# Kernel optimization log

Measured on AMD Instinct MI355X. Metric: run time of the kernel, lower is better.

Reference implementation:

```python
import jax, jax.numpy as jnp
import numpy as np

N = 100000   # nodes
E = 1600000  # edges
DIN, H, DOUT = 128, 64, 40
EPS = 1e-5

def setup_inputs() -> dict:
    key = jax.random.key(0)
    ks = jax.random.split(key, 8)
    def w(k, fan_in, shape):
        return jax.random.normal(k, shape, jnp.float32) * (1.0 / np.sqrt(fan_in))
    return {
        "node_feat": jax.random.normal(ks[0], (N, DIN), jnp.float32),
        "edge_index": jax.random.randint(ks[1], (2, E), 0, N, dtype=jnp.int32),
        "W1": w(ks[2], DIN, (DIN, H)), "b1": jnp.zeros((H,), jnp.float32),
        "g1": jnp.ones((H,), jnp.float32), "beta1": jnp.zeros((H,), jnp.float32),
        "W2": w(ks[3], H, (H, H)), "b2": jnp.zeros((H,), jnp.float32),
        "g2": jnp.ones((H,), jnp.float32), "beta2": jnp.zeros((H,), jnp.float32),
        "W3": w(ks[4], H, (H, H)), "b3": jnp.zeros((H,), jnp.float32),
        "Wf": w(ks[5], H, (H, DOUT)), "bf": jnp.zeros((DOUT,), jnp.float32),
    }

def _gcn_conv(x, src, dst, norm, W, b):
    # x: [N, Cin] -> linear then D^{-1/2}(A+I)D^{-1/2} aggregation (PyG GCNConv)
    h = x @ W                              # [N, Cout]
    msg = h[src] * norm[:, None]           # [E+N, Cout] gather + scale
    return jax.ops.segment_sum(msg, dst, num_segments=N) + b

def _bn(x, g, b):
    # BatchNorm1d over node dim with batch statistics (biased var)
    m = jnp.mean(x, axis=0)
    v = jnp.mean((x - m) ** 2, axis=0)
    return (x - m) * jax.lax.rsqrt(v + EPS) * g + b

def reference(node_feat, edge_index, W1, b1, g1, beta1, W2, b2, g2, beta2, W3, b3, Wf, bf):
    loop = jnp.arange(N, dtype=edge_index.dtype)
    src = jnp.concatenate([edge_index[0], loop])   # add self loops
    dst = jnp.concatenate([edge_index[1], loop])
    deg = jax.ops.segment_sum(jnp.ones_like(src, dtype=node_feat.dtype), dst, num_segments=N)
    dis = jax.lax.rsqrt(deg)                        # deg >= 1 (self loops)
    norm = dis[src] * dis[dst]                      # [E+N]

    x1 = jax.nn.relu(_bn(_gcn_conv(node_feat, src, dst, norm, W1, b1), g1, beta1))
    # dropout is identity in eval mode
    x2 = jax.nn.relu(_bn(_gcn_conv(x1, src, dst, norm, W2, b2), g2, beta2))
    x3 = _gcn_conv(x2, src, dst, norm, W3, b3)

    x = jnp.max(jnp.stack([x1, x2, x3], axis=0), axis=0)  # JumpingKnowledge 'max'
    return x @ Wf + bf
```

## Files before the change

kernel.cpp:

```cpp
#include <hip/hip_runtime.h>

#define NN 100000
#define NE 1600000
#define DIN 128
#define HDIM 64
#define DOUT 40
#define EPS 1e-5f
#define NXCD 8
#define CAP 64

typedef int int4v __attribute__((ext_vector_type(4)));
typedef float f4v __attribute__((ext_vector_type(4)));

__device__ __forceinline__ float bf2f(unsigned short v) {
    return __uint_as_float(((unsigned int)v) << 16);
}
__device__ __forceinline__ unsigned short f2bf(float f) {
    unsigned int u = __float_as_uint(f);
    u += 0x7FFFu + ((u >> 16) & 1u);
    return (unsigned short)(u >> 16);
}

__device__ __forceinline__ int ntl(const int* p) { return __builtin_nontemporal_load(p); }
__device__ __forceinline__ int4v ntl4(const int4v* p) { return __builtin_nontemporal_load(p); }
__device__ __forceinline__ f4v ntlf4(const f4v* p) { return __builtin_nontemporal_load(p); }

__global__ __launch_bounds__(256) void fill_kernel(const int* __restrict__ ei,
                                                   int* __restrict__ cnt,
                                                   int* __restrict__ esrc) {
    const int xcd = blockIdx.x & (NXCD - 1);
    const int lo = xcd * (NN / NXCD);
    const int hi = (xcd == NXCD - 1) ? NN : lo + (NN / NXCD);
    const int slot = blockIdx.x >> 3;
    const int nslot = gridDim.x >> 3;
    const int4v* d4 = (const int4v*)(ei + NE);
    for (int e4 = slot * blockDim.x + threadIdx.x; e4 < NE / 4; e4 += nslot * blockDim.x) {
        int4v d = ntl4(d4 + e4);
#pragma unroll
        for (int k = 0; k < 4; ++k) {
            int dd = d[k];
            if (dd >= lo && dd < hi) {
                int pos = atomicAdd(&cnt[dd], 1);
                if (pos < CAP) {
                    int s = ntl(ei + 4 * e4 + k);
                    __builtin_nontemporal_store(s, &esrc[(dd << 6) + pos]);
                }
            }
        }
    }
}

__global__ __launch_bounds__(256) void dis_kernel(const int* __restrict__ cnt,
                                                  float* __restrict__ dis) {
    for (int i = blockIdx.x * blockDim.x + threadIdx.x; i < NN; i += gridDim.x * blockDim.x)
        dis[i] = rsqrtf((float)(cnt[i] + 1));
}

template <int K, int TR, bool BN, bool NTL>
__global__ __launch_bounds__(256) void gemm_lds(const float* __restrict__ x,
                                                const float* __restrict__ W,
                                                const float* __restrict__ dis,
                                                const float* __restrict__ sc,
                                                const float* __restrict__ sh,
                                                unsigned short* __restrict__ h2) {
    __shared__ float xs[TR][K];
    const int tid = threadIdx.x;
    const int lane = tid & 63;
    const int wv = tid >> 6;
    float w[K];
#pragma unroll
    for (int k = 0; k < K; ++k) w[k] = W[k * 64 + lane];

    float4 scv, shv;
    if (BN) {
        const int c4 = tid & (K / 4 - 1);
        scv = ((const float4*)sc)[c4];
        shv = ((const float4*)sh)[c4];
    }

    const int row0 = blockIdx.x * TR;
    const int remRows = NN - row0;
    const int nvec = ((remRows >= TR) ? TR : remRows) * K / 4;
    const f4v* srcv = (const f4v*)(x + (long long)row0 * K);
    f4v* dstv = (f4v*)&xs[0][0];
    for (int i = tid; i < nvec; i += 256) {
        f4v v = NTL ? ntlf4(srcv + i) : srcv[i];
        if (BN) {
            v.x = fmaxf(fmaf(v.x, scv.x, shv.x), 0.f);
            v.y = fmaxf(fmaf(v.y, scv.y, shv.y), 0.f);
            v.z = fmaxf(fmaf(v.z, scv.z, shv.z), 0.f);
            v.w = fmaxf(fmaf(v.w, scv.w, shv.w), 0.f);
        }
        dstv[i] = v;
    }
    __syncthreads();

    const int rpw = TR / 4;
#pragma unroll
    for (int rr = 0; rr < rpw; ++rr) {
        const int r = wv * rpw + rr;
        const int row = row0 + r;
        if (row >= NN) break;
        float a0 = 0.f, a1 = 0.f, a2 = 0.f, a3 = 0.f;
#pragma unroll
        for (int k = 0; k < K; k += 4) {
            float4 xv = *(const float4*)&xs[r][k];
            a0 = fmaf(xv.x, w[k + 0], a0);
            a1 = fmaf(xv.y, w[k + 1], a1);
            a2 = fmaf(xv.z, w[k + 2], a2);
            a3 = fmaf(xv.w, w[k + 3], a3);
        }
        h2[row * 64 + lane] = f2bf(((a0 + a1) + (a2 + a3)) * dis[row]);
    }
}

__global__ __launch_bounds__(256) void agg_csr(const int* __restrict__ cnt,
                                               const int* __restrict__ esrc,
                                               const float* __restrict__ dis,
                                               const unsigned short* __restrict__ h2,
                                               float* __restrict__ y) {
    const int tid = threadIdx.x;
    const int wv = tid >> 6;
    const int lane = tid & 63;
    const int half = lane >> 5;
    const int c = lane & 31;
    const int node = blockIdx.x * 8 + wv * 2 + half;
    const ushort2* h2v = (const ushort2*)h2;
    ushort2 p0 = h2v[node * 32 + c];
    float ax = bf2f(p0.x), ay = bf2f(p0.y);
    const int deg = min(cnt[node], CAP);
    const int m = max(deg, __shfl_xor(deg, 32));
    const int jb = node << 6;
#pragma unroll 8
    for (int t = 0; t < m; ++t) {
        int sv = esrc[jb + t];
        int s = (t < deg) ? sv : NN;
        ushort2 p = h2v[s * 32 + c];
        ax += bf2f(p.x);
        ay += bf2f(p.y);
    }
    float dn = dis[node];
    ((float2*)(y + node * 64))[c] = make_float2(ax * dn, ay * dn);
}

__global__ __launch_bounds__(256) void agg_final(const int* __restrict__ cnt,
                                                 const int* __restrict__ esrc,
                                                 const float* __restrict__ dis,
                                                 const unsigned short* __restrict__ h2,
                                                 const float* __restrict__ x1,
                                                 const float* __restrict__ x2,
                                                 const float* __restrict__ sc1,
                                                 const float* __restrict__ sh1,
                                                 const float* __restrict__ sc2,
                                                 const float* __restrict__ sh2,
                                                 const float* __restrict__ b3,
                                                 const float* __restrict__ Wf,
                                                 const float* __restrict__ bf,
                                                 float* __restrict__ out) {
    __shared__ float m[8][64];
    const int tid = threadIdx.x;
    const int wv = tid >> 6;
    const int lane = tid & 63;
    const int half = lane >> 5;
    const int c = lane & 31;
    const int node = blockIdx.x * 8 + wv * 2 + half;
    const ushort2* h2v = (const ushort2*)h2;
    ushort2 p0 = h2v[node * 32 + c];
    float ax = bf2f(p0.x), ay = bf2f(p0.y);
    const int deg = min(cnt[node], CAP);
    const int mm = max(deg, __shfl_xor(deg, 32));
    const int jb = node << 6;
#pragma unroll 8
    for (int t = 0; t < mm; ++t) {
        int sv = esrc[jb + t];
        int s = (t < deg) ? sv : NN;
        ushort2 p = h2v[s * 32 + c];
        ax += bf2f(p.x);
        ay += bf2f(p.y);
    }
    const float dn = dis[node];
    const int c0 = 2 * c;
    const int o = node * 64 + c0;
    float2 x1v = *(const float2*)(x1 + o);
    float2 x2v = *(const float2*)(x2 + o);
    float v3x = fmaf(ax, dn, b3[c0]);
    float v3y = fmaf(ay, dn, b3[c0 + 1]);
    float v1x = fmaxf(fmaf(x1v.x, sc1[c0], sh1[c0]), 0.f);
    float v1y = fmaxf(fmaf(x1v.y, sc1[c0 + 1], sh1[c0 + 1]), 0.f);
    float v2x = fmaxf(fmaf(x2v.x, sc2[c0], sh2[c0]), 0.f);
    float v2y = fmaxf(fmaf(x2v.y, sc2[c0 + 1], sh2[c0 + 1]), 0.f);
    const int rl = wv * 2 + half;
    m[rl][c0] = fmaxf(fmaxf(v1x, v2x), v3x);
    m[rl][c0 + 1] = fmaxf(fmaxf(v1y, v2y), v3y);
    __syncthreads();
#pragma unroll
    for (int rr = wv; rr < 8; rr += 4) {
        if (lane < DOUT) {
            float a2 = bf[lane];
#pragma unroll
            for (int k = 0; k < 64; ++k) a2 += m[rr][k] * Wf[k * DOUT + lane];
            out[(blockIdx.x * 8 + rr) * DOUT + lane] = a2;
        }
    }
}

__global__ __launch_bounds__(256) void stats_kernel(const float* __restrict__ y, float* stats) {
    const int tid = threadIdx.x;
    const int c = tid & 63, rg = tid >> 6;
    float s = 0.f, s2 = 0.f;
    for (int row = blockIdx.x * 4 + rg; row < NN; row += gridDim.x * 4) {
        float v = y[row * 64 + c];
        s += v;
        s2 += v * v;
    }
    __shared__ float ls[256], ls2[256];
    ls[tid] = s; ls2[tid] = s2;
    __syncthreads();
    if (tid < 64) {
        s = ls[tid] + ls[tid + 64] + ls[tid + 128] + ls[tid + 192];
        s2 = ls2[tid] + ls2[tid + 64] + ls2[tid + 128] + ls2[tid + 192];
        atomicAdd(&stats[tid], s);
        atomicAdd(&stats[64 + tid], s2);
    }
}

__global__ __launch_bounds__(64) void bn_coef(const float* __restrict__ stats,
                                              const float* __restrict__ g,
                                              const float* __restrict__ beta,
                                              float* __restrict__ sc,
                                              float* __restrict__ sh) {
    const int c = threadIdx.x;
    const float invN = 1.0f / NN;
    float m = stats[c] * invN;
    float var = stats[64 + c] * invN - m * m;
    float s = g[c] * rsqrtf(var + EPS);
    sc[c] = s;
    sh[c] = beta[c] - m * s;
}

extern "C" void kernel_launch(void* const* d_in, const int* in_sizes, int n_in,
                              void* d_out, int out_size, void* d_ws, size_t ws_size,
                              hipStream_t stream) {
    const float* node_feat = (const float*)d_in[0];
    const int*   ei        = (const int*)d_in[1];
    const float* W1 = (const float*)d_in[2];
    const float* g1 = (const float*)d_in[4];
    const float* beta1 = (const float*)d_in[5];
    const float* W2 = (const float*)d_in[6];
    const float* g2 = (const float*)d_in[8];
    const float* beta2 = (const float*)d_in[9];
    const float* W3 = (const float*)d_in[10];
    const float* b3 = (const float*)d_in[11];
    const float* Wf = (const float*)d_in[12];
    const float* bf = (const float*)d_in[13];
    float* out = (float*)d_out;

    float* ws  = (float*)d_ws;
    float* dis = ws;
    unsigned short* h2 = (unsigned short*)(dis + NN);
    float* x1  = (float*)(h2 + (NN + 1) * 64);
    float* x2  = x1 + NN * 64;
    float* stats = x2 + NN * 64;
    float* sc1 = stats + 128;
    float* sh1 = sc1 + 64;
    float* sc2 = sh1 + 64;
    float* sh2 = sc2 + 64;
    int* cnt  = (int*)(sh2 + 64);
    int* esrc = cnt + NN;

    const int B = 256;
    const int gElem = 2048;
    const int gAgg = NN / 8;

    hipMemsetAsync(cnt, 0, NN * sizeof(int), stream);
    hipMemsetAsync(h2 + NN * 64, 0, 64 * sizeof(unsigned short), stream);
    fill_kernel<<<gElem, B, 0, stream>>>(ei, cnt, esrc);
    dis_kernel<<<512, B, 0, stream>>>(cnt, dis);

    gemm_lds<DIN, 32, false, true><<<(NN + 31) / 32, B, 0, stream>>>(node_feat, W1, dis, nullptr, nullptr, h2);
    agg_csr<<<gAgg, B, 0, stream>>>(cnt, esrc, dis, h2, x1);
    hipMemsetAsync(stats, 0, 128 * sizeof(float), stream);
    stats_kernel<<<512, B, 0, stream>>>(x1, stats);
    bn_coef<<<1, 64, 0, stream>>>(stats, g1, beta1, sc1, sh1);

    gemm_lds<HDIM, 64, true, false><<<(NN + 63) / 64, B, 0, stream>>>(x1, W2, dis, sc1, sh1, h2);
    agg_csr<<<gAgg, B, 0, stream>>>(cnt, esrc, dis, h2, x2);
    hipMemsetAsync(stats, 0, 128 * sizeof(float), stream);
    stats_kernel<<<512, B, 0, stream>>>(x2, stats);
    bn_coef<<<1, 64, 0, stream>>>(stats, g2, beta2, sc2, sh2);

    gemm_lds<HDIM, 64, true, false><<<(NN + 63) / 64, B, 0, stream>>>(x2, W3, dis, sc2, sh2, h2);
    agg_final<<<gAgg, B, 0, stream>>>(cnt, esrc, dis, h2, x1, x2,
                                      sc1, sh1, sc2, sh2, b3, Wf, bf, out);
}
```

Baseline: 428.7 us.

## Shard bf16 feature table into four column slices to shrink gather working set

The GEMM now writes h2 as four separate 16-column shards, and the aggregation kernels run four blocks per node group, each gathering only one shard. Each block's random gathers then touch a table a quarter the size, which is meant to improve cache hit rates (L2/MALL) for the irregular neighbour reads. The fused final layer is split out into a separate JK-max kernel that writes a jk buffer and a final projection kernel. The cost is more blocks that each re-read the edge lists (four times the index traffic) and an extra round trip through jk in memory.

```diff
diff --git a/kernel.cpp b/kernel.cpp
--- a/kernel.cpp
+++ b/kernel.cpp
@@ -8,6 +8,8 @@
 #define EPS 1e-5f
 #define NXCD 8
 #define CAP 64
+#define NSH 4
+#define SSTR ((NN + 1) * 16)
 
 typedef int int4v __attribute__((ext_vector_type(4)));
 typedef float f4v __attribute__((ext_vector_type(4)));
@@ -95,6 +97,7 @@
     }
     __syncthreads();
 
+    unsigned short* hout = h2 + (lane >> 4) * SSTR + (lane & 15);
     const int rpw = TR / 4;
 #pragma unroll
     for (int rr = 0; rr < rpw; ++rr) {
@@ -110,7 +113,7 @@
             a2 = fmaf(xv.z, w[k + 2], a2);
             a3 = fmaf(xv.w, w[k + 3], a3);
         }
-        h2[row * 64 + lane] = f2bf(((a0 + a1) + (a2 + a3)) * dis[row]);
+        hout[row * 16] = f2bf(((a0 + a1) + (a2 + a3)) * dis[row]);
     }
 }
 
@@ -120,87 +123,98 @@
                                                const unsigned short* __restrict__ h2,
                                                float* __restrict__ y) {
     const int tid = threadIdx.x;
+    const int g = blockIdx.x & (NSH - 1);
+    const int blk = blockIdx.x >> 2;
     const int wv = tid >> 6;
     const int lane = tid & 63;
-    const int half = lane >> 5;
-    const int c = lane & 31;
-    const int node = blockIdx.x * 8 + wv * 2 + half;
-    const ushort2* h2v = (const ushort2*)h2;
-    ushort2 p0 = h2v[node * 32 + c];
+    const int node = blk * 32 + wv * 8 + (lane >> 3);
+    const int cp = lane & 7;
+    const ushort2* hv = (const ushort2*)(h2 + g * SSTR);
+    ushort2 p0 = hv[node * 8 + cp];
     float ax = bf2f(p0.x), ay = bf2f(p0.y);
     const int deg = min(cnt[node], CAP);
-    const int m = max(deg, __shfl_xor(deg, 32));
+    int m = deg;
+    m = max(m, __shfl_xor(m, 8));
+    m = max(m, __shfl_xor(m, 16));
+    m = max(m, __shfl_xor(m, 32));
     const int jb = node << 6;
 #pragma unroll 8
     for (int t = 0; t < m; ++t) {
         int sv = esrc[jb + t];
         int s = (t < deg) ? sv : NN;
-        ushort2 p = h2v[s * 32 + c];
+        ushort2 p = hv[s * 8 + cp];
         ax += bf2f(p.x);
         ay += bf2f(p.y);
     }
     float dn = dis[node];
-    ((float2*)(y + node * 64))[c] = make_float2(ax * dn, ay * dn);
-}
-
-__global__ __launch_bounds__(256) void agg_final(const int* __restrict__ cnt,
-                                                 const int* __restrict__ esrc,
-                                                 const float* __restrict__ dis,
-                                                 const unsigned short* __restrict__ h2,
-                                                 const float* __restrict__ x1,
-                                                 const float* __restrict__ x2,
-                                                 const float* __restrict__ sc1,
-                                                 const float* __restrict__ sh1,
-                                                 const float* __restrict__ sc2,
-                                                 const float* __restrict__ sh2,
-                                                 const float* __restrict__ b3,
-                                                 const float* __restrict__ Wf,
-                                                 const float* __restrict__ bf,
-                                                 float* __restrict__ out) {
-    __shared__ float m[8][64];
-    const int tid = threadIdx.x;
+    ((float2*)(y + node * 64))[g * 8 + cp] = make_float2(ax * dn, ay * dn);
+}
+
+__global__ __launch_bounds__(256) void agg3_jk(const int* __restrict__ cnt,
+                                               const int* __restrict__ esrc,
+                                               const float* __restrict__ dis,
+                                               const unsigned short* __restrict__ h2,
+                                               const float* __restrict__ x1,
+                                               const float* __restrict__ x2,
+                                               const float* __restrict__ sc1,
+                                               const float* __restrict__ sh1,
+                                               const float* __restrict__ sc2,
+                                               const float* __restrict__ sh2,
+                                               const float* __restrict__ b3,
+                                               float* __restrict__ jk) {
+    const int tid = threadIdx.x;
+    const int g = blockIdx.x & (NSH - 1);
+    const int blk = blockIdx.x >> 2;
     const int wv = tid >> 6;
     const int lane = tid & 63;
-    const int half = lane >> 5;
-    const int c = lane & 31;
-    const int node = blockIdx.x * 8 + wv * 2 + half;
-    const ushort2* h2v = (const ushort2*)h2;
-    ushort2 p0 = h2v[node * 32 + c];
+    const int node = blk * 32 + wv * 8 + (lane >> 3);
+    const int cp = lane & 7;
+    const ushort2* hv = (const ushort2*)(h2 + g * SSTR);
+    ushort2 p0 = hv[node * 8 + cp];
     float ax = bf2f(p0.x), ay = bf2f(p0.y);
     const int deg = min(cnt[node], CAP);
-    const int mm = max(deg, __shfl_xor(deg, 32));
+    int m = deg;
+    m = max(m, __shfl_xor(m, 8));
+    m = max(m, __shfl_xor(m, 16));
+    m = max(m, __shfl_xor(m, 32));
     const int jb = node << 6;
 #pragma unroll 8
-    for (int t = 0; t < mm; ++t) {
+    for (int t = 0; t < m; ++t) {
         int sv = esrc[jb + t];
         int s = (t < deg) ? sv : NN;
-        ushort2 p = h2v[s * 32 + c];
+        ushort2 p = hv[s * 8 + cp];
         ax += bf2f(p.x);
         ay += bf2f(p.y);
     }
     const float dn = dis[node];
-    const int c0 = 2 * c;
-    const int o = node * 64 + c0;
-    float2 x1v = *(const float2*)(x1 + o);
-    float2 x2v = *(const float2*)(x2 + o);
+    const int c0 = g * 16 + cp * 2;
+    float2 x1v = ((const float2*)(x1 + node * 64))[g * 8 + cp];
+    float2 x2v = ((const float2*)(x2 + node * 64))[g * 8 + cp];
     float v3x = fmaf(ax, dn, b3[c0]);
     float v3y = fmaf(ay, dn, b3[c0 + 1]);
     float v1x = fmaxf(fmaf(x1v.x, sc1[c0], sh1[c0]), 0.f);
     float v1y = fmaxf(fmaf(x1v.y, sc1[c0 + 1], sh1[c0 + 1]), 0.f);
     float v2x = fmaxf(fmaf(x2v.x, sc2[c0], sh2[c0]), 0.f);
     float v2y = fmaxf(fmaf(x2v.y, sc2[c0 + 1], sh2[c0 + 1]), 0.f);
-    const int rl = wv * 2 + half;
-    m[rl][c0] = fmaxf(fmaxf(v1x, v2x), v3x);
-    m[rl][c0 + 1] = fmaxf(fmaxf(v1y, v2y), v3y);
+    ((float2*)(jk + node * 64))[g * 8 + cp] =
+        make_float2(fmaxf(fmaxf(v1x, v2x), v3x), fmaxf(fmaxf(v1y, v2y), v3y));
+}
+
+__global__ __launch_bounds__(256) void final_kernel(const float* __restrict__ jk,
+                                                    const float* __restrict__ Wf,
+                                                    const float* __restrict__ bf,
+                                                    float* __restrict__ out) {
+    __shared__ float m[4][64];
+    const int tid = threadIdx.x;
+    const int r = tid >> 6, c = tid & 63;
+    const int row = blockIdx.x * 4 + r;
+    m[r][c] = jk[row * 64 + c];
     __syncthreads();
-#pragma unroll
-    for (int rr = wv; rr < 8; rr += 4) {
-        if (lane < DOUT) {
-            float a2 = bf[lane];
-#pragma unroll
-            for (int k = 0; k < 64; ++k) a2 += m[rr][k] * Wf[k * DOUT + lane];
-            out[(blockIdx.x * 8 + rr) * DOUT + lane] = a2;
-        }
+    if (c < DOUT) {
+        float acc = bf[c];
+#pragma unroll
+        for (int k = 0; k < 64; ++k) acc += m[r][k] * Wf[k * DOUT + c];
+        out[row * DOUT + c] = acc;
     }
 }
 
@@ -258,9 +272,10 @@
     float* ws  = (float*)d_ws;
     float* dis = ws;
     unsigned short* h2 = (unsigned short*)(dis + NN);
-    float* x1  = (float*)(h2 + (NN + 1) * 64);
+    float* x1  = (float*)(h2 + NSH * SSTR);
     float* x2  = x1 + NN * 64;
-    float* stats = x2 + NN * 64;
+    float* jk  = x2 + NN * 64;
+    float* stats = jk + NN * 64;
     float* sc1 = stats + 128;
     float* sh1 = sc1 + 64;
     float* sc2 = sh1 + 64;
@@ -270,10 +285,12 @@
 
     const int B = 256;
     const int gElem = 2048;
-    const int gAgg = NN / 8;
+    const int gAgg = (NN / 32) * NSH;
+    const int gFin = NN / 4;
 
     hipMemsetAsync(cnt, 0, NN * sizeof(int), stream);
-    hipMemsetAsync(h2 + NN * 64, 0, 64 * sizeof(unsigned short), stream);
+    for (int g = 0; g < NSH; ++g)
+        hipMemsetAsync(h2 + g * SSTR + NN * 16, 0, 16 * sizeof(unsigned short), stream);
     fill_kernel<<<gElem, B, 0, stream>>>(ei, cnt, esrc);
     dis_kernel<<<512, B, 0, stream>>>(cnt, dis);
 
@@ -290,6 +307,7 @@
     bn_coef<<<1, 64, 0, stream>>>(stats, g2, beta2, sc2, sh2);
 
     gemm_lds<HDIM, 64, true, false><<<(NN + 63) / 64, B, 0, stream>>>(x2, W3, dis, sc2, sh2, h2);
-    agg_final<<<gAgg, B, 0, stream>>>(cnt, esrc, dis, h2, x1, x2,
-                                      sc1, sh1, sc2, sh2, b3, Wf, bf, out);
-}
+    agg3_jk<<<gAgg, B, 0, stream>>>(cnt, esrc, dis, h2, x1, x2,
+                                    sc1, sh1, sc2, sh2, b3, jk);
+    final_kernel<<<gFin, B, 0, stream>>>(jk, Wf, bf, out);
+}
```

Result: slower. 491.3 us (+14.6%).
